# Performance work log

Measured on AMD Instinct MI355X. Metric: run time of the kernel, lower is better.

## Reference

```python
import jax, jax.numpy as jnp
import numpy as np

G = 4        # split_group
H = 64       # hidden_size_t = 256 // 4 (causal -> //1)
I = 64       # input_size_t  = 256 // 4
EPS = 1e-5


def _lstm(x, W_ih, W_hh, b):
    """Grouped unidirectional LSTM, PyTorch gate order (i,f,g,o).
    x: (G,B,T,I); W_ih: (G,4H,I); W_hh: (G,4H,H); b: (G,4H) -> (G,B,T,H)"""
    g, bsz, t, _ = x.shape
    h_dim = W_hh.shape[-1]
    # precompute input projections for all timesteps
    xp = jnp.einsum('gbti,gki->gbtk', x, W_ih) + b[:, None, None, :]  # (G,B,T,4H)
    xp = jnp.moveaxis(xp, 2, 0)  # (T,G,B,4H)

    def step(carry, xt):
        h, c = carry
        gates = xt + jnp.einsum('gbh,gkh->gbk', h, W_hh)
        i_g, f_g, g_g, o_g = jnp.split(gates, 4, axis=-1)
        i_g = jax.nn.sigmoid(i_g)
        f_g = jax.nn.sigmoid(f_g)
        g_g = jnp.tanh(g_g)
        o_g = jax.nn.sigmoid(o_g)
        c = f_g * c + i_g * g_g
        h = o_g * jnp.tanh(c)
        return (h, c), h

    h0 = jnp.zeros((g, bsz, h_dim), x.dtype)
    _, hs = jax.lax.scan(step, (h0, h0), xp)  # hs: (T,G,B,H)
    return jnp.moveaxis(hs, 0, 2)  # (G,B,T,H)


def _bn(x, gamma, beta):
    """BatchNorm1d (training stats) over (B,T) per feature. x: (B,T,F)"""
    mean = x.mean(axis=(0, 1))
    var = x.var(axis=(0, 1))
    return (x - mean) * jax.lax.rsqrt(var + EPS) * gamma + beta


def setup_inputs() -> dict:
    key = jax.random.key(0)
    ks = jax.random.split(key, 12)
    s = 0.1
    F = G * H
    return {
        'inpt': jax.random.normal(ks[0], (32, 1000, 256), jnp.float32),
        'W_ih1': jax.random.normal(ks[1], (G, 4 * H, I), jnp.float32) * s,
        'W_hh1': jax.random.normal(ks[2], (G, 4 * H, H), jnp.float32) * s,
        'b1': jax.random.normal(ks[3], (G, 4 * H), jnp.float32) * s,
        'W_ih2': jax.random.normal(ks[4], (G, 4 * H, H), jnp.float32) * s,
        'W_hh2': jax.random.normal(ks[5], (G, 4 * H, H), jnp.float32) * s,
        'b2': jax.random.normal(ks[6], (G, 4 * H), jnp.float32) * s,
        'gamma1': jnp.ones((F,), jnp.float32) + jax.random.normal(ks[7], (F,)) * 0.01,
        'beta1': jax.random.normal(ks[8], (F,), jnp.float32) * 0.01,
        'gamma2': jnp.ones((F,), jnp.float32) + jax.random.normal(ks[9], (F,)) * 0.01,
        'beta2': jax.random.normal(ks[10], (F,), jnp.float32) * 0.01,
    }


def reference(inpt, W_ih1, W_hh1, b1, W_ih2, W_hh2, b2, gamma1, beta1, gamma2, beta2):
    B, T, F = inpt.shape
    # chunk along features -> (G,B,T,I)
    xg = jnp.transpose(inpt.reshape(B, T, G, I), (2, 0, 1, 3))
    y1 = _lstm(xg, W_ih1, W_hh1, b1)  # (G,B,T,H)
    # torch.stack(dim=-1) + flatten: feature index = h*G + g (interleaved)
    x = jnp.transpose(y1, (1, 2, 3, 0)).reshape(B, T, H * G)
    x = _bn(x, gamma1, beta1)
    # chunk again into G contiguous groups of size H
    xg2 = jnp.transpose(x.reshape(B, T, G, H), (2, 0, 1, 3))
    y2 = _lstm(xg2, W_ih2, W_hh2, b2)  # (G,B,T,H)
    # torch.cat(dim=-1): contiguous groups
    x = jnp.transpose(y2, (1, 2, 0, 3)).reshape(B, T, G * H)
    x = _bn(x, gamma2, beta2)
    return x
```

## Files before the change

kernel.cpp:

```cpp
#include <hip/hip_runtime.h>
#include <math.h>

#define G 4
#define H 64
#define T 1000
#define B 32
#define ROWS (B*T)

__device__ __forceinline__ float sigm(float x) {
    return 1.f / (1.f + __expf(-x));
}
__device__ __forceinline__ float tanh_f(float x) {
    return 2.f / (1.f + __expf(-2.f * x)) - 1.f;
}

template<bool BN>
__global__ __launch_bounds__(256)
void xp_proj(const float* __restrict__ xin,
             const float* __restrict__ Wih,
             const float* __restrict__ bias,
             const float* __restrict__ ac,
             float* __restrict__ xp,
             int t0, int tcn, int tcmax, int TT)
{
    int id = blockIdx.x;
    const int kt = id & 3; id >>= 2;
    const int tt = id % TT; id /= TT;
    const int b = id & 31;
    const int g = id >> 5;

    __shared__ __align__(16) float xs[64][68];
    __shared__ __align__(16) float ws[64][68];

    const int tx = threadIdx.x & 15, ty = threadIdx.x >> 4;

    #pragma unroll
    for (int j = 0; j < 4; ++j) {
        int idx = j * 1024 + threadIdx.x * 4;
        int r = idx >> 6, ci = idx & 63;
        float4 v = *(const float4*)&Wih[(size_t)((g * 256 + kt * 64 + r) << 6) + ci];
        *(float4*)&ws[r][ci] = v;
    }
    #pragma unroll
    for (int j = 0; j < 4; ++j) {
        int idx = j * 1024 + threadIdx.x * 4;
        int r = idx >> 6, ci = idx & 63;
        int tg = t0 + tt * 64 + r; if (tg > T - 1) tg = T - 1;
        float4 v = *(const float4*)&xin[((size_t)b * T + tg) * 256 + g * 64 + ci];
        if (BN) {
            float4 a4 = *(const float4*)&ac[g * 64 + ci];
            float4 c4 = *(const float4*)&ac[256 + g * 64 + ci];
            v.x = fmaf(v.x, a4.x, c4.x);
            v.y = fmaf(v.y, a4.y, c4.y);
            v.z = fmaf(v.z, a4.z, c4.z);
            v.w = fmaf(v.w, a4.w, c4.w);
        }
        *(float4*)&xs[r][ci] = v;
    }
    __syncthreads();

    float acc[4][4] = {};
    #pragma unroll
    for (int i4 = 0; i4 < 16; ++i4) {
        float4 xv[4], wv[4];
        #pragma unroll
        for (int q = 0; q < 4; ++q) xv[q] = *(const float4*)&xs[ty * 4 + q][i4 * 4];
        #pragma unroll
        for (int q = 0; q < 4; ++q) wv[q] = *(const float4*)&ws[tx * 4 + q][i4 * 4];
        #pragma unroll
        for (int a = 0; a < 4; ++a)
            #pragma unroll
            for (int c = 0; c < 4; ++c) {
                acc[a][c] = fmaf(xv[a].x, wv[c].x, acc[a][c]);
                acc[a][c] = fmaf(xv[a].y, wv[c].y, acc[a][c]);
                acc[a][c] = fmaf(xv[a].z, wv[c].z, acc[a][c]);
                acc[a][c] = fmaf(xv[a].w, wv[c].w, acc[a][c]);
            }
    }

    const int kbase = kt * 64 + tx * 4;
    const float4 b4 = *(const float4*)&bias[g * 256 + kbase];
    float* xpb = xp + (size_t)(g * 32 + b) * tcmax * 256;
    #pragma unroll
    for (int a = 0; a < 4; ++a) {
        int tloc = tt * 64 + ty * 4 + a;
        if (tloc < tcn) {
            float4 o;
            o.x = acc[a][0] + b4.x;
            o.y = acc[a][1] + b4.y;
            o.z = acc[a][2] + b4.z;
            o.w = acc[a][3] + b4.w;
            *(float4*)&xpb[(size_t)tloc * 256 + kbase] = o;
        }
    }
}

template<int LAYER>
__global__ __launch_bounds__(256, 1)
void rec_xp(const float* __restrict__ xp,
            const float* __restrict__ Whh,
            float* __restrict__ out,
            float* __restrict__ stateh, float* __restrict__ statec,
            int t0, int t1, int tcmax)
{
    const int blk = blockIdx.x;
    const int g = blk & 3, b = blk >> 2;
    const int l  = threadIdx.x & 63;
    const int w  = threadIdx.x >> 6;
    const int gt = l >> 4, c16 = l & 15;
    const int col = w * 16 + c16;
    const int row = gt * 64 + col;

    __shared__ __align__(16) float hsh[2][64];

    float whh[64];
    {
        const float4* wp = (const float4*)&Whh[(size_t)((g * 256 + row) << 6)];
        #pragma unroll
        for (int i = 0; i < 16; ++i) {
            float4 v = wp[i];
            whh[4*i] = v.x; whh[4*i+1] = v.y; whh[4*i+2] = v.z; whh[4*i+3] = v.w;
        }
    }
    const float m  = (gt == 2) ? 2.f : 1.f;
    const float A  = (gt == 2) ? 2.f : 1.f;
    const float Bc = (gt == 2) ? -1.f : 0.f;

    float cst;
    if (t0 == 0) {
        cst = 0.f;
        if (threadIdx.x < 64) hsh[0][threadIdx.x] = 0.f;
    } else {
        cst = statec[blk * 64 + col];
        if (threadIdx.x < 64) hsh[0][threadIdx.x] = stateh[blk * 64 + threadIdx.x];
    }

    const float* xpb = xp + (size_t)(g * 32 + b) * tcmax * 256 + row;
    float p[4];
    #pragma unroll
    for (int j = 0; j < 4; ++j) {
        int tp = t0 + j; if (tp > t1 - 1) tp = t1 - 1;
        p[j] = xpb[(size_t)(tp - t0) * 256];
    }
    __syncthreads();

    float hl = 0.f;
    const int nsteps = t1 - t0;
    for (int s = 0; s < nsteps; s += 4) {
        #pragma unroll
        for (int j = 0; j < 4; ++j) {
            const int cur = j & 1;
            float a0 = 0.f, a1 = 0.f, a2 = 0.f, a3 = 0.f;
            const float4* hv = (const float4*)hsh[cur];
            #pragma unroll
            for (int q = 0; q < 16; ++q) {
                float4 z = hv[q];
                a0 = fmaf(whh[4*q],   z.x, a0);
                a1 = fmaf(whh[4*q+1], z.y, a1);
                a2 = fmaf(whh[4*q+2], z.z, a2);
                a3 = fmaf(whh[4*q+3], z.w, a3);
            }
            float acc = p[j] + ((a0 + a1) + (a2 + a3));
            {
                int tp = t0 + s + j + 4; if (tp > t1 - 1) tp = t1 - 1;
                p[j] = xpb[(size_t)(tp - t0) * 256];
            }
            float act = A / (1.f + __expf(-m * acc)) + Bc;
            float ig = __shfl(act, c16);
            float fg = __shfl(act, c16 + 16);
            float gg = __shfl(act, c16 + 32);
            float og = __shfl(act, c16 + 48);
            cst = fmaf(fg, cst, ig * gg);
            float h = og * tanh_f(cst);
            if (gt == 0) {
                hsh[cur ^ 1][col] = h;
                int t = t0 + s + j;
                if (LAYER == 1) out[((size_t)b * T + t) * 256 + col * 4 + g] = h;
                else            out[((size_t)b * T + t) * 256 + g * 64 + col] = h;
            }
            hl = h;
            __syncthreads();
        }
    }
    if (gt == 0) {
        stateh[blk * 64 + col] = hl;
        statec[blk * 64 + col] = cst;
    }
}

template<int LAYER>
__global__ __launch_bounds__(256, 1)
void rec_kernel(const float* __restrict__ xin,
                const float* __restrict__ Wih,
                const float* __restrict__ Whh,
                const float* __restrict__ bias,
                const float* __restrict__ bnac,
                float* __restrict__ out)
{
    const int g = blockIdx.x & 3;
    const int b = blockIdx.x >> 2;
    const int k = threadIdx.x;

    __shared__ __align__(16) float xsh[2][64];
    __shared__ __align__(16) float hsh[64];
    __shared__ __align__(16) float gsh[256];

    float wih[64], whh[64];
    {
        const float4* wi = (const float4*)(Wih + (size_t)(g * 256 + k) * 64);
        const float4* wh = (const float4*)(Whh + (size_t)(g * 256 + k) * 64);
        #pragma unroll
        for (int i = 0; i < 16; ++i) {
            float4 v = wi[i];
            wih[4*i] = v.x; wih[4*i+1] = v.y; wih[4*i+2] = v.z; wih[4*i+3] = v.w;
            float4 u = wh[i];
            whh[4*i] = u.x; whh[4*i+1] = u.y; whh[4*i+2] = u.z; whh[4*i+3] = u.w;
        }
    }
    const float bk = bias[g * 256 + k];
    const long rowbase = (long)b * T;
    const int  colbase = g * 64;

    float c = 0.f, af = 1.f, cf = 0.f;
    float xa = 0.f, xb = 0.f;

    if (k < 64) {
        if (LAYER == 2) { af = bnac[colbase + k]; cf = bnac[256 + colbase + k]; }
        hsh[k] = 0.f;
        float x0 = xin[(rowbase + 0) * 256 + colbase + k];
        xsh[0][k] = (LAYER == 2) ? fmaf(x0, af, cf) : x0;
        xa = xin[(rowbase + 1) * 256 + colbase + k];
        xb = xin[(rowbase + 2) * 256 + colbase + k];
    }
    __syncthreads();

    for (int t = 0; t < T; ++t) {
        const int cur = t & 1;
        float xn = 0.f;
        if (k < 64) {
            int tp = t + 3; if (tp > T - 1) tp = T - 1;
            xn = xin[(rowbase + tp) * 256 + colbase + k];
        }
        const float* xs = xsh[cur];
        float a0 = 0.f, a1 = 0.f, a2 = 0.f, a3 = 0.f;
        #pragma unroll
        for (int i = 0; i < 64; i += 4) {
            a0 = fmaf(wih[i],     xs[i],     a0);
            a1 = fmaf(wih[i + 1], xs[i + 1], a1);
            a2 = fmaf(wih[i + 2], xs[i + 2], a2);
            a3 = fmaf(wih[i + 3], xs[i + 3], a3);
        }
        #pragma unroll
        for (int jq = 0; jq < 64; jq += 4) {
            a0 = fmaf(whh[jq],     hsh[jq],     a0);
            a1 = fmaf(whh[jq + 1], hsh[jq + 1], a1);
            a2 = fmaf(whh[jq + 2], hsh[jq + 2], a2);
            a3 = fmaf(whh[jq + 3], hsh[jq + 3], a3);
        }
        const float acc = bk + ((a0 + a1) + (a2 + a3));
        const float act = (k >= 128 && k < 192) ? tanh_f(acc) : sigm(acc);
        gsh[k] = act;
        __syncthreads();

        if (k < 64) {
            const float ig = gsh[k];
            const float fg = gsh[64 + k];
            const float gg = gsh[128 + k];
            const float og = gsh[192 + k];
            c = fmaf(fg, c, ig * gg);
            const float h = og * tanh_f(c);
            hsh[k] = h;
            const long rrow = rowbase + t;
            if (LAYER == 1) out[rrow * 256 + k * 4 + g] = h;
            else            out[rrow * 256 + colbase + k] = h;
            xsh[cur ^ 1][k] = fmaf(xa, af, cf);
            xa = xb; xb = xn;
        }
        __syncthreads();
    }
}

__global__ void zero_ws(float* sums) {
    int i = blockIdx.x * blockDim.x + threadIdx.x;
    if (i < 512) sums[i] = 0.f;
}

__global__ __launch_bounds__(256) void stats_reduce(const float* __restrict__ x,
                                                    float* __restrict__ sums)
{
    float s = 0.f, ss = 0.f;
    for (int r = blockIdx.x; r < ROWS; r += gridDim.x) {
        float v = x[(long)r * 256 + threadIdx.x];
        s += v;
        ss = fmaf(v, v, ss);
    }
    atomicAdd(&sums[threadIdx.x], s);
    atomicAdd(&sums[256 + threadIdx.x], ss);
}

__global__ void stats_finalize(const float* __restrict__ sums,
                               const float* __restrict__ gamma,
                               const float* __restrict__ beta,
                               float* __restrict__ ac)
{
    int f = threadIdx.x;
    const float invN = 1.f / (float)ROWS;
    float mean = sums[f] * invN;
    float var  = fmaf(-mean, mean, sums[256 + f] * invN);
    float a = gamma[f] * rsqrtf(var + 1e-5f);
    ac[f]       = a;
    ac[256 + f] = fmaf(-mean, a, beta[f]);
}

__global__ __launch_bounds__(256) void bn_apply(float* __restrict__ x,
                                                const float* __restrict__ ac)
{
    __shared__ float a_s[256], c_s[256];
    a_s[threadIdx.x] = ac[threadIdx.x];
    c_s[threadIdx.x] = ac[256 + threadIdx.x];
    __syncthreads();
    const long n4 = (long)ROWS * 64;
    for (long i = (long)blockIdx.x * blockDim.x + threadIdx.x; i < n4;
         i += (long)gridDim.x * blockDim.x) {
        float4 v = ((float4*)x)[i];
        int f0 = (int)((i * 4) & 255);
        v.x = fmaf(v.x, a_s[f0],     c_s[f0]);
        v.y = fmaf(v.y, a_s[f0 + 1], c_s[f0 + 1]);
        v.z = fmaf(v.z, a_s[f0 + 2], c_s[f0 + 2]);
        v.w = fmaf(v.w, a_s[f0 + 3], c_s[f0 + 3]);
        ((float4*)x)[i] = v;
    }
}

extern "C" void kernel_launch(void* const* d_in, const int* in_sizes, int n_in,
                              void* d_out, int out_size, void* d_ws, size_t ws_size,
                              hipStream_t stream)
{
    const float* inpt   = (const float*)d_in[0];
    const float* Wih1   = (const float*)d_in[1];
    const float* Whh1   = (const float*)d_in[2];
    const float* b1     = (const float*)d_in[3];
    const float* Wih2   = (const float*)d_in[4];
    const float* Whh2   = (const float*)d_in[5];
    const float* b2     = (const float*)d_in[6];
    const float* gamma1 = (const float*)d_in[7];
    const float* beta1  = (const float*)d_in[8];
    const float* gamma2 = (const float*)d_in[9];
    const float* beta2  = (const float*)d_in[10];
    float* out  = (float*)d_out;

    float* sums = (float*)d_ws;
    float* acbn = sums + 512;
    float* sth  = acbn + 512;
    float* stc  = sth + 8192;
    float* xpb  = stc + 8192;

    const size_t fixedB = (size_t)(512 + 512 + 8192 + 8192) * 4;
    long availT = ((long)ws_size - (long)fixedB) / (128L * 256L * 4L);
    int Tcmax = (availT >= T) ? T : (int)(availT & ~3L);

    if (Tcmax >= 100) {
        zero_ws<<<2, 256, 0, stream>>>(sums);
        for (int t0 = 0; t0 < T; t0 += Tcmax) {
            int tcn = T - t0; if (tcn > Tcmax) tcn = Tcmax;
            int TT = (tcn + 63) / 64;
            xp_proj<false><<<128 * TT * 4, 256, 0, stream>>>(
                inpt, Wih1, b1, nullptr, xpb, t0, tcn, Tcmax, TT);
            rec_xp<1><<<128, 256, 0, stream>>>(xpb, Whh1, out, sth, stc, t0, t0 + tcn, Tcmax);
        }
        stats_reduce<<<256, 256, 0, stream>>>(out, sums);
        stats_finalize<<<1, 256, 0, stream>>>(sums, gamma1, beta1, acbn);

        for (int t0 = 0; t0 < T; t0 += Tcmax) {
            int tcn = T - t0; if (tcn > Tcmax) tcn = Tcmax;
            int TT = (tcn + 63) / 64;
            xp_proj<true><<<128 * TT * 4, 256, 0, stream>>>(
                out, Wih2, b2, acbn, xpb, t0, tcn, Tcmax, TT);
            rec_xp<2><<<128, 256, 0, stream>>>(xpb, Whh2, out, sth, stc, t0, t0 + tcn, Tcmax);
        }
        zero_ws<<<2, 256, 0, stream>>>(sums);
        stats_reduce<<<256, 256, 0, stream>>>(out, sums);
        stats_finalize<<<1, 256, 0, stream>>>(sums, gamma2, beta2, acbn);
        bn_apply<<<2048, 256, 0, stream>>>(out, acbn);
    } else {
        zero_ws<<<2, 256, 0, stream>>>(sums);
        rec_kernel<1><<<G * B, 256, 0, stream>>>(inpt, Wih1, Whh1, b1, nullptr, out);
        stats_reduce<<<256, 256, 0, stream>>>(out, sums);
        stats_finalize<<<1, 256, 0, stream>>>(sums, gamma1, beta1, acbn);
        rec_kernel<2><<<G * B, 256, 0, stream>>>(out, Wih2, Whh2, b2, acbn, out);
        zero_ws<<<2, 256, 0, stream>>>(sums);
        stats_reduce<<<256, 256, 0, stream>>>(out, sums);
        stats_finalize<<<1, 256, 0, stream>>>(sums, gamma2, beta2, acbn);
        bn_apply<<<2048, 256, 0, stream>>>(out, acbn);
    }
}
```

Baseline: 1.691 ms.

## Split recurrent matvec across 512 threads, fuse BN stats, reuse x tile in projection

The recurrent kernel now uses 512 threads per block: each gate row's 64-element dot product is split in half across lanes and combined with a shuffle-xor. Gate combination is done with xor shuffles instead of indexed shuffles, which halves per-thread weight registers and shortens the serial per-step latency. BatchNorm sum and sum-of-squares are accumulated inside the recurrent kernel and added with atomics, which removes the separate stats_reduce passes. The input projection kernel now loops over all four gate tiles per block so the x tile is loaded once, at the cost of four times fewer blocks.

```diff
diff --git a/kernel.cpp b/kernel.cpp
--- a/kernel.cpp
+++ b/kernel.cpp
@@ -24,7 +24,6 @@
              int t0, int tcn, int tcmax, int TT)
 {
     int id = blockIdx.x;
-    const int kt = id & 3; id >>= 2;
     const int tt = id % TT; id /= TT;
     const int b = id & 31;
     const int g = id >> 5;
@@ -34,13 +33,6 @@
 
     const int tx = threadIdx.x & 15, ty = threadIdx.x >> 4;
 
-    #pragma unroll
-    for (int j = 0; j < 4; ++j) {
-        int idx = j * 1024 + threadIdx.x * 4;
-        int r = idx >> 6, ci = idx & 63;
-        float4 v = *(const float4*)&Wih[(size_t)((g * 256 + kt * 64 + r) << 6) + ci];
-        *(float4*)&ws[r][ci] = v;
-    }
     #pragma unroll
     for (int j = 0; j < 4; ++j) {
         int idx = j * 1024 + threadIdx.x * 4;
@@ -57,67 +49,82 @@
         }
         *(float4*)&xs[r][ci] = v;
     }
-    __syncthreads();
-
-    float acc[4][4] = {};
-    #pragma unroll
-    for (int i4 = 0; i4 < 16; ++i4) {
-        float4 xv[4], wv[4];
-        #pragma unroll
-        for (int q = 0; q < 4; ++q) xv[q] = *(const float4*)&xs[ty * 4 + q][i4 * 4];
-        #pragma unroll
-        for (int q = 0; q < 4; ++q) wv[q] = *(const float4*)&ws[tx * 4 + q][i4 * 4];
-        #pragma unroll
-        for (int a = 0; a < 4; ++a)
+
+    float* xpb = xp + (size_t)(g * 32 + b) * tcmax * 256;
+
+    for (int kt = 0; kt < 4; ++kt) {
+        __syncthreads();
+        #pragma unroll
+        for (int j = 0; j < 4; ++j) {
+            int idx = j * 1024 + threadIdx.x * 4;
+            int r = idx >> 6, ci = idx & 63;
+            float4 v = *(const float4*)&Wih[(size_t)((g * 256 + kt * 64 + r) << 6) + ci];
+            *(float4*)&ws[r][ci] = v;
+        }
+        __syncthreads();
+
+        float acc[4][4] = {};
+        #pragma unroll
+        for (int i4 = 0; i4 < 16; ++i4) {
+            float4 xv[4], wv[4];
             #pragma unroll
-            for (int c = 0; c < 4; ++c) {
-                acc[a][c] = fmaf(xv[a].x, wv[c].x, acc[a][c]);
-                acc[a][c] = fmaf(xv[a].y, wv[c].y, acc[a][c]);
-                acc[a][c] = fmaf(xv[a].z, wv[c].z, acc[a][c]);
-                acc[a][c] = fmaf(xv[a].w, wv[c].w, acc[a][c]);
+            for (int q = 0; q < 4; ++q) xv[q] = *(const float4*)&xs[ty * 4 + q][i4 * 4];
+            #pragma unroll
+            for (int q = 0; q < 4; ++q) wv[q] = *(const float4*)&ws[tx * 4 + q][i4 * 4];
+            #pragma unroll
+            for (int a = 0; a < 4; ++a)
+                #pragma unroll
+                for (int c = 0; c < 4; ++c) {
+                    acc[a][c] = fmaf(xv[a].x, wv[c].x, acc[a][c]);
+                    acc[a][c] = fmaf(xv[a].y, wv[c].y, acc[a][c]);
+                    acc[a][c] = fmaf(xv[a].z, wv[c].z, acc[a][c]);
+                    acc[a][c] = fmaf(xv[a].w, wv[c].w, acc[a][c]);
+                }
+        }
+
+        const int kbase = kt * 64 + tx * 4;
+        const float4 b4 = *(const float4*)&bias[g * 256 + kbase];
+        #pragma unroll
+        for (int a = 0; a < 4; ++a) {
+            int tloc = tt * 64 + ty * 4 + a;
+            if (tloc < tcn) {
+                float4 o;
+                o.x = acc[a][0] + b4.x;
+                o.y = acc[a][1] + b4.y;
+                o.z = acc[a][2] + b4.z;
+                o.w = acc[a][3] + b4.w;
+                *(float4*)&xpb[(size_t)tloc * 256 + kbase] = o;
             }
-    }
-
-    const int kbase = kt * 64 + tx * 4;
-    const float4 b4 = *(const float4*)&bias[g * 256 + kbase];
-    float* xpb = xp + (size_t)(g * 32 + b) * tcmax * 256;
-    #pragma unroll
-    for (int a = 0; a < 4; ++a) {
-        int tloc = tt * 64 + ty * 4 + a;
-        if (tloc < tcn) {
-            float4 o;
-            o.x = acc[a][0] + b4.x;
-            o.y = acc[a][1] + b4.y;
-            o.z = acc[a][2] + b4.z;
-            o.w = acc[a][3] + b4.w;
-            *(float4*)&xpb[(size_t)tloc * 256 + kbase] = o;
         }
     }
 }
 
 template<int LAYER>
-__global__ __launch_bounds__(256, 1)
+__global__ __launch_bounds__(512, 1)
 void rec_xp(const float* __restrict__ xp,
             const float* __restrict__ Whh,
             float* __restrict__ out,
             float* __restrict__ stateh, float* __restrict__ statec,
+            float* __restrict__ sums,
             int t0, int t1, int tcmax)
 {
     const int blk = blockIdx.x;
-    const int g = blk & 3, b = blk >> 2;
-    const int l  = threadIdx.x & 63;
-    const int w  = threadIdx.x >> 6;
-    const int gt = l >> 4, c16 = l & 15;
-    const int col = w * 16 + c16;
+    const int g = blk >> 5, b = blk & 31;
+    const int tid = threadIdx.x;
+    const int w = tid >> 6, l = tid & 63;
+    const int c8 = l & 7;
+    const int jh = (l >> 3) & 1;
+    const int gt = l >> 4;
+    const int col = w * 8 + c8;
     const int row = gt * 64 + col;
 
     __shared__ __align__(16) float hsh[2][64];
 
-    float whh[64];
+    float whh[32];
     {
-        const float4* wp = (const float4*)&Whh[(size_t)((g * 256 + row) << 6)];
-        #pragma unroll
-        for (int i = 0; i < 16; ++i) {
+        const float4* wp = (const float4*)&Whh[(size_t)((g * 256 + row) << 6) + jh * 32];
+        #pragma unroll
+        for (int i = 0; i < 8; ++i) {
             float4 v = wp[i];
             whh[4*i] = v.x; whh[4*i+1] = v.y; whh[4*i+2] = v.z; whh[4*i+3] = v.w;
         }
@@ -129,61 +136,70 @@
     float cst;
     if (t0 == 0) {
         cst = 0.f;
-        if (threadIdx.x < 64) hsh[0][threadIdx.x] = 0.f;
+        if (tid < 64) hsh[0][tid] = 0.f;
     } else {
         cst = statec[blk * 64 + col];
-        if (threadIdx.x < 64) hsh[0][threadIdx.x] = stateh[blk * 64 + threadIdx.x];
-    }
-
-    const float* xpb = xp + (size_t)(g * 32 + b) * tcmax * 256 + row;
+        if (tid < 64) hsh[0][tid] = stateh[blk * 64 + tid];
+    }
+
+    const float* xpb = xp + (size_t)blk * tcmax * 256 + row;
     float p[4];
     #pragma unroll
     for (int j = 0; j < 4; ++j) {
         int tp = t0 + j; if (tp > t1 - 1) tp = t1 - 1;
         p[j] = xpb[(size_t)(tp - t0) * 256];
     }
+
+    float hl = 0.f, st_s = 0.f, st_ss = 0.f;
     __syncthreads();
 
-    float hl = 0.f;
     const int nsteps = t1 - t0;
-    for (int s = 0; s < nsteps; s += 4) {
+    for (int s4 = 0; s4 < nsteps; s4 += 4) {
         #pragma unroll
         for (int j = 0; j < 4; ++j) {
             const int cur = j & 1;
             float a0 = 0.f, a1 = 0.f, a2 = 0.f, a3 = 0.f;
-            const float4* hv = (const float4*)hsh[cur];
+            const float4* hv = (const float4*)&hsh[cur][jh * 32];
             #pragma unroll
-            for (int q = 0; q < 16; ++q) {
+            for (int q = 0; q < 8; ++q) {
                 float4 z = hv[q];
                 a0 = fmaf(whh[4*q],   z.x, a0);
                 a1 = fmaf(whh[4*q+1], z.y, a1);
                 a2 = fmaf(whh[4*q+2], z.z, a2);
                 a3 = fmaf(whh[4*q+3], z.w, a3);
             }
-            float acc = p[j] + ((a0 + a1) + (a2 + a3));
+            float acc = (a0 + a1) + (a2 + a3);
+            float full = acc + __shfl_xor(acc, 8);
+            float pre = full + p[j];
             {
-                int tp = t0 + s + j + 4; if (tp > t1 - 1) tp = t1 - 1;
+                int tp = t0 + s4 + j + 4; if (tp > t1 - 1) tp = t1 - 1;
                 p[j] = xpb[(size_t)(tp - t0) * 256];
             }
-            float act = A / (1.f + __expf(-m * acc)) + Bc;
-            float ig = __shfl(act, c16);
-            float fg = __shfl(act, c16 + 16);
-            float gg = __shfl(act, c16 + 32);
-            float og = __shfl(act, c16 + 48);
-            cst = fmaf(fg, cst, ig * gg);
-            float h = og * tanh_f(cst);
-            if (gt == 0) {
+            float act = A / (1.f + __expf(-m * pre)) + Bc;
+            float P = act * __shfl_xor(act, 32);
+            float Q = __shfl_xor(P, 16);
+            cst = fmaf(act, cst, Q);
+            float R = __shfl_xor(cst, 32);
+            float h = act * tanh_f(R);
+            if (gt == 3 && jh == 0) {
                 hsh[cur ^ 1][col] = h;
-                int t = t0 + s + j;
+                int t = t0 + s4 + j;
                 if (LAYER == 1) out[((size_t)b * T + t) * 256 + col * 4 + g] = h;
                 else            out[((size_t)b * T + t) * 256 + g * 64 + col] = h;
+                st_s += h;
+                st_ss = fmaf(h, h, st_ss);
+                hl = h;
             }
-            hl = h;
             __syncthreads();
         }
     }
-    if (gt == 0) {
+    if (gt == 3 && jh == 0) {
         stateh[blk * 64 + col] = hl;
+        int f = (LAYER == 1) ? (col * 4 + g) : (g * 64 + col);
+        atomicAdd(&sums[f], st_s);
+        atomicAdd(&sums[256 + f], st_ss);
+    }
+    if (gt == 1 && jh == 0) {
         statec[blk * 64 + col] = cst;
     }
 }
@@ -280,9 +296,9 @@
     }
 }
 
-__global__ void zero_ws(float* sums) {
+__global__ void zero_ws(float* sums, int n) {
     int i = blockIdx.x * blockDim.x + threadIdx.x;
-    if (i < 512) sums[i] = 0.f;
+    if (i < n) sums[i] = 0.f;
 }
 
 __global__ __launch_bounds__(256) void stats_reduce(const float* __restrict__ x,
@@ -349,48 +365,50 @@
     const float* beta2  = (const float*)d_in[10];
     float* out  = (float*)d_out;
 
-    float* sums = (float*)d_ws;
-    float* acbn = sums + 512;
-    float* sth  = acbn + 512;
-    float* stc  = sth + 8192;
-    float* xpb  = stc + 8192;
-
-    const size_t fixedB = (size_t)(512 + 512 + 8192 + 8192) * 4;
+    float* sums1 = (float*)d_ws;
+    float* sums2 = sums1 + 512;
+    float* acbn1 = sums2 + 512;
+    float* acbn2 = acbn1 + 512;
+    float* sth   = acbn2 + 512;
+    float* stc   = sth + 8192;
+    float* xpb   = stc + 8192;
+
+    const size_t fixedB = (size_t)(4 * 512 + 2 * 8192) * 4;
     long availT = ((long)ws_size - (long)fixedB) / (128L * 256L * 4L);
     int Tcmax = (availT >= T) ? T : (int)(availT & ~3L);
 
     if (Tcmax >= 100) {
-        zero_ws<<<2, 256, 0, stream>>>(sums);
+        zero_ws<<<4, 256, 0, stream>>>(sums1, 1024);
+
         for (int t0 = 0; t0 < T; t0 += Tcmax) {
             int tcn = T - t0; if (tcn > Tcmax) tcn = Tcmax;
             int TT = (tcn + 63) / 64;
-            xp_proj<false><<<128 * TT * 4, 256, 0, stream>>>(
+            xp_proj<false><<<128 * TT, 256, 0, stream>>>(
                 inpt, Wih1, b1, nullptr, xpb, t0, tcn, Tcmax, TT);
-            rec_xp<1><<<128, 256, 0, stream>>>(xpb, Whh1, out, sth, stc, t0, t0 + tcn, Tcmax);
-        }
-        stats_reduce<<<256, 256, 0, stream>>>(out, sums);
-        stats_finalize<<<1, 256, 0, stream>>>(sums, gamma1, beta1, acbn);
+            rec_xp<1><<<128, 512, 0, stream>>>(xpb, Whh1, out, sth, stc, sums1,
+                                               t0, t0 + tcn, Tcmax);
+        }
+        stats_finalize<<<1, 256, 0, stream>>>(sums1, gamma1, beta1, acbn1);
 
         for (int t0 = 0; t0 < T; t0 += Tcmax) {
             int tcn = T - t0; if (tcn > Tcmax) tcn = Tcmax;
             int TT = (tcn + 63) / 64;
-            xp_proj<true><<<128 * TT * 4, 256, 0, stream>>>(
-                out, Wih2, b2, acbn, xpb, t0, tcn, Tcmax, TT);
-            rec_xp<2><<<128, 256, 0, stream>>>(xpb, Whh2, out, sth, stc, t0, t0 + tcn, Tcmax);
-        }
-        zero_ws<<<2, 256, 0, stream>>>(sums);
-        stats_reduce<<<256, 256, 0, stream>>>(out, sums);
-        stats_finalize<<<1, 256, 0, stream>>>(sums, gamma2, beta2, acbn);
-        bn_apply<<<2048, 256, 0, stream>>>(out, acbn);
+            xp_proj<true><<<128 * TT, 256, 0, stream>>>(
+                out, Wih2, b2, acbn1, xpb, t0, tcn, Tcmax, TT);
+            rec_xp<2><<<128, 512, 0, stream>>>(xpb, Whh2, out, sth, stc, sums2,
+                                               t0, t0 + tcn, Tcmax);
+        }
+        stats_finalize<<<1, 256, 0, stream>>>(sums2, gamma2, beta2, acbn2);
+        bn_apply<<<2048, 256, 0, stream>>>(out, acbn2);
     } else {
-        zero_ws<<<2, 256, 0, stream>>>(sums);
+        zero_ws<<<2, 256, 0, stream>>>(sums1, 512);
         rec_kernel<1><<<G * B, 256, 0, stream>>>(inpt, Wih1, Whh1, b1, nullptr, out);
-        stats_reduce<<<256, 256, 0, stream>>>(out, sums);
-        stats_finalize<<<1, 256, 0, stream>>>(sums, gamma1, beta1, acbn);
-        rec_kernel<2><<<G * B, 256, 0, stream>>>(out, Wih2, Whh2, b2, acbn, out);
-        zero_ws<<<2, 256, 0, stream>>>(sums);
-        stats_reduce<<<256, 256, 0, stream>>>(out, sums);
-        stats_finalize<<<1, 256, 0, stream>>>(sums, gamma2, beta2, acbn);
-        bn_apply<<<2048, 256, 0, stream>>>(out, acbn);
-    }
-}
+        stats_reduce<<<256, 256, 0, stream>>>(out, sums1);
+        stats_finalize<<<1, 256, 0, stream>>>(sums1, gamma1, beta1, acbn1);
+        rec_kernel<2><<<G * B, 256, 0, stream>>>(out, Wih2, Whh2, b2, acbn1, out);
+        zero_ws<<<2, 256, 0, stream>>>(sums2, 512);
+        stats_reduce<<<256, 256, 0, stream>>>(out, sums2);
+        stats_finalize<<<1, 256, 0, stream>>>(sums2, gamma2, beta2, acbn2);
+        bn_apply<<<2048, 256, 0, stream>>>(out, acbn2);
+    }
+}
```

Result: faster. 1.536 ms (-9.1%).
